# Performance work log

Hardware: AMD Instinct MI355X
Metric: run time of the kernel (lower is better)

## Reference

```python
import jax, jax.numpy as jnp
import numpy as np

N_NODES = 4096
IN_FEAT = 256
N_HEADS = 8
N_HIDDEN = 64  # out_features // n_heads
NEG_SLOPE = 0.2
EDGE_PROB = 0.05


def setup_inputs() -> dict:
    key = jax.random.key(0)
    k1, k2, k3, k4 = jax.random.split(key, 4)
    h = jax.random.normal(k1, (N_NODES, IN_FEAT), dtype=jnp.float32)
    # binary adjacency mask [N, N, 1] (broadcast over heads), as in the torch asserts
    adj_mat = (jax.random.uniform(k2, (N_NODES, N_NODES, 1)) < EDGE_PROB).astype(jnp.float32)
    # nn.Linear(in_features, n_heads*n_hidden, bias=False) weight: [H*F, in]
    W = jax.random.normal(k3, (N_HEADS * N_HIDDEN, IN_FEAT), dtype=jnp.float32) / np.sqrt(IN_FEAT)
    # nn.Linear(2*n_hidden, 1, bias=False) weight, flattened: [2*F]
    a = jax.random.normal(k4, (2 * N_HIDDEN,), dtype=jnp.float32) / np.sqrt(2 * N_HIDDEN)
    return {"h": h, "adj_mat": adj_mat, "W": W, "a": a}


def reference(h, adj_mat, W, a):
    n = h.shape[0]
    # g: [N, H, F]
    g = (h @ W.T).reshape(n, N_HEADS, N_HIDDEN)
    # attn(cat[g_i, g_j]) == a_l . g_i + a_r . g_j  (linear, no bias)
    a_l = a[:N_HIDDEN]
    a_r = a[N_HIDDEN:]
    el = jnp.einsum('ihf,f->ih', g, a_l)  # [N, H]
    er = jnp.einsum('jhf,f->jh', g, a_r)  # [N, H]
    e = jax.nn.leaky_relu(el[:, None, :] + er[None, :, :], NEG_SLOPE)  # [N, N, H]
    # note: original multiplies scores by adjacency (not masked_fill)
    e = e * adj_mat  # adj broadcasts over heads
    att = jax.nn.softmax(e, axis=1)  # softmax over source nodes j
    # dropout is identity at eval (dropout_rate=0.0)
    out = jnp.einsum('ijh,jhf->ihf', att, g)  # [N, H, F]
    return out.reshape(n, N_HEADS * N_HIDDEN)
```

## Files before the change

kernel.cpp:

```cpp
#include <hip/hip_runtime.h>

#define N_NODES 4096
#define IN_FEAT 256
#define N_HEADS 8
#define N_HIDDEN 64
#define OUT_FEAT (N_HEADS * N_HIDDEN)
#define NEG_SLOPE 0.2f

typedef _Float16 half8 __attribute__((ext_vector_type(8)));
typedef _Float16 h2 __attribute__((ext_vector_type(2)));
typedef float floatx4 __attribute__((ext_vector_type(4)));

__global__ __launch_bounds__(256) void produce(
    const float* __restrict__ H, const float* __restrict__ adj,
    const float* __restrict__ Wt, const float* __restrict__ a,
    _Float16* __restrict__ GT16, float* __restrict__ elT,
    _Float16* __restrict__ eR1h, _Float16* __restrict__ eR2h,
    unsigned long long* __restrict__ bits) {
  __shared__ _Float16 SM[4 * 64 * 64];
  const int t = threadIdx.x;
  const int bx = blockIdx.x, by = blockIdx.y;

  if (by >= 8) {
    const int c = bx * 8 + (by - 8);
    const size_t W0 = (size_t)c * 512;
    const int wv = t >> 6, lane = t & 63;
    for (int k0 = 0; k0 < 128; k0 += 8) {
      float v[8];
#pragma unroll
      for (int k = 0; k < 8; ++k)
        v[k] = adj[(W0 + wv * 128 + k0 + k) * 64 + lane];
#pragma unroll
      for (int k = 0; k < 8; ++k) {
        unsigned long long m = __ballot(v[k] != 0.f);
        if (lane == 0) bits[W0 + wv * 128 + k0 + k] = m;
      }
    }
    return;
  }

  _Float16* Ah = SM;
  _Float16* Al = SM + 4096;
  _Float16* Bh = SM + 8192;
  _Float16* Bl = SM + 12288;
  const int w = t >> 6, l = t & 63;
  const int n16 = l & 15, q = l >> 4;
  const int bi = bx, bo = by;
  const int m0 = bi * 64 + w * 16;

  floatx4 acc[4];
#pragma unroll
  for (int ct = 0; ct < 4; ++ct) acc[ct] = (floatx4)0.f;

  for (int kc = 0; kc < 4; ++kc) {
    if (kc) __syncthreads();
#pragma unroll
    for (int p = 0; p < 4; ++p) {
      const int idx = p * 256 + t;
      const int r = idx >> 4;
      const int c4 = (idx & 15) << 2;
      const int dst = r * 64 + ((((idx & 15) >> 1)) ^ (r & 7)) * 8 + (idx & 1) * 4;
      float4 hv = *(const float4*)(H + (size_t)(bi * 64 + r) * IN_FEAT + kc * 64 + c4);
      float4 wv = *(const float4*)(Wt + (size_t)(bo * 64 + r) * IN_FEAT + kc * 64 + c4);
      union { _Float16 h[4]; int2 d; } hh_, hl_, wh_, wl_;
      hh_.h[0] = (_Float16)hv.x; hh_.h[1] = (_Float16)hv.y;
      hh_.h[2] = (_Float16)hv.z; hh_.h[3] = (_Float16)hv.w;
      hl_.h[0] = (_Float16)(hv.x - (float)hh_.h[0]);
      hl_.h[1] = (_Float16)(hv.y - (float)hh_.h[1]);
      hl_.h[2] = (_Float16)(hv.z - (float)hh_.h[2]);
      hl_.h[3] = (_Float16)(hv.w - (float)hh_.h[3]);
      wh_.h[0] = (_Float16)wv.x; wh_.h[1] = (_Float16)wv.y;
      wh_.h[2] = (_Float16)wv.z; wh_.h[3] = (_Float16)wv.w;
      wl_.h[0] = (_Float16)(wv.x - (float)wh_.h[0]);
      wl_.h[1] = (_Float16)(wv.y - (float)wh_.h[1]);
      wl_.h[2] = (_Float16)(wv.z - (float)wh_.h[2]);
      wl_.h[3] = (_Float16)(wv.w - (float)wh_.h[3]);
      *(int2*)&Ah[dst] = hh_.d;
      *(int2*)&Al[dst] = hl_.d;
      *(int2*)&Bh[dst] = wh_.d;
      *(int2*)&Bl[dst] = wl_.d;
    }
    __syncthreads();
#pragma unroll
    for (int ks = 0; ks < 2; ++ks) {
      const int ao = (w * 16 + n16) * 64 + (((ks << 2) + q) ^ (n16 & 7)) * 8;
      half8 Afh = *(const half8*)&Ah[ao];
      half8 Afl = *(const half8*)&Al[ao];
#pragma unroll
      for (int ct = 0; ct < 4; ++ct) {
        const int bofs = (ct * 16 + n16) * 64 + (((ks << 2) + q) ^ (n16 & 7)) * 8;
        half8 Bfh = *(const half8*)&Bh[bofs];
        half8 Bfl = *(const half8*)&Bl[bofs];
        acc[ct] = __builtin_amdgcn_mfma_f32_16x16x32_f16(Afh, Bfh, acc[ct], 0, 0, 0);
        acc[ct] = __builtin_amdgcn_mfma_f32_16x16x32_f16(Afl, Bfh, acc[ct], 0, 0, 0);
        acc[ct] = __builtin_amdgcn_mfma_f32_16x16x32_f16(Afh, Bfl, acc[ct], 0, 0, 0);
      }
    }
  }

  float aLv[4], aRv[4];
#pragma unroll
  for (int ct = 0; ct < 4; ++ct) {
    aLv[ct] = a[ct * 16 + n16];
    aRv[ct] = a[64 + ct * 16 + n16];
  }
#pragma unroll
  for (int reg = 0; reg < 4; ++reg) {
    float sl = 0.f, sr = 0.f;
#pragma unroll
    for (int ct = 0; ct < 4; ++ct) {
      sl = fmaf(acc[ct][reg], aLv[ct], sl);
      sr = fmaf(acc[ct][reg], aRv[ct], sr);
    }
#pragma unroll
    for (int off = 1; off < 16; off <<= 1) {
      sl += __shfl_xor(sl, off);
      sr += __shfl_xor(sr, off);
    }
    if (n16 == 0) {
      const int rowi = m0 + q * 4 + reg;
      elT[(size_t)bo * N_NODES + rowi] = sl;
      eR1h[(size_t)bo * N_NODES + rowi] = (_Float16)__expf(sr);
      eR2h[(size_t)bo * N_NODES + rowi] = (_Float16)__expf(0.2f * sr);
    }
  }

  __syncthreads();
  _Float16* LG = SM;
#pragma unroll
  for (int ct = 0; ct < 4; ++ct)
#pragma unroll
    for (int reg = 0; reg < 4; ++reg)
      LG[(w * 16 + q * 4 + reg) * 72 + ct * 16 + n16] = (_Float16)acc[ct][reg];
  __syncthreads();
  {
    const int f = t >> 2, jq = t & 3;
    union { _Float16 hh[16]; int4 v[2]; } u;
#pragma unroll
    for (int k = 0; k < 16; ++k) u.hh[k] = LG[(jq * 16 + k) * 72 + f];
    _Float16* dst = GT16 + (size_t)(bo * 64 + f) * N_NODES + bi * 64 + jq * 16;
    *(int4*)dst = u.v[0];
    *(int4*)(dst + 8) = u.v[1];
  }
}

__global__ __launch_bounds__(256) void attn_v8(
    const unsigned long long* __restrict__ bits, const _Float16* __restrict__ GT16,
    const float* __restrict__ elT, const _Float16* __restrict__ eR1h,
    const _Float16* __restrict__ eR2h, float* __restrict__ out) {
  __shared__ __align__(16) _Float16 Gt[2][2][4096];
  __shared__ __align__(16) _Float16 eRs1[2][2][64];
  __shared__ __align__(16) _Float16 eRs2[2][2][64];
  __shared__ float eL1s[32], eL2s[32];
  __shared__ float Zh1[32], Zfull[32];

  const int t = threadIdx.x;
  const int ib = blockIdx.x, h = blockIdx.y;
  const int i0 = ib * 32;
  const int w = t >> 6, l = t & 63, n16 = l & 15, q = l >> 4;
  const int rt = w & 1, jh = w >> 1;

  const _Float16* gsrcs[4];
  int ldsbase[4];
#pragma unroll
  for (int c = 0; c < 4; ++c) {
    const int flat = w * 256 + c * 64 + l;
    const int fjh = flat >> 9;
    const int ff = (flat >> 3) & 63;
    const int ss = flat & 7;
    const int cg = ss ^ (ff & 7);
    gsrcs[c] = GT16 + (size_t)(h * 64 + ff) * N_NODES + fjh * 2048 + cg * 8;
    ldsbase[c] = (w * 256 + c * 64) * 8;
  }
  const int era = (t >> 3) & 1, erjh = t >> 4, erseg = t & 7;
  const _Float16* esrc0 = (era ? eR2h : eR1h) + (size_t)h * N_NODES + erjh * 2048 + erseg * 8;
  const unsigned long long* bp = bits + (size_t)(i0 + rt * 16 + n16) * 64 + jh * 32;

  if (t < 32) {
    float e = elT[(size_t)h * N_NODES + i0 + t];
    eL1s[t] = __expf(e);
    eL2s[t] = __expf(0.2f * e);
  }
#pragma unroll
  for (int c = 0; c < 4; ++c)
    __builtin_amdgcn_global_load_lds(
        (const __attribute__((address_space(1))) unsigned int*)gsrcs[c],
        (__attribute__((address_space(3))) unsigned int*)(&Gt[0][0][0] + ldsbase[c]),
        16, 0, 0);
  if (t < 32) {
    int4 ev = *(const int4*)esrc0;
    *(int4*)&(era ? eRs2 : eRs1)[0][erjh][erseg * 8] = ev;
  }
  unsigned long long bvc = bp[0];
  __syncthreads();

  const _Float16 e1f = (_Float16)eL1s[rt * 16 + n16];
  const _Float16 e2f = (_Float16)eL2s[rt * 16 + n16];
  const h2 eL1h2 = {e1f, e1f};
  const h2 eL2h2 = {e2f, e2f};
  half8 Bones;
#pragma unroll
  for (int k = 0; k < 8; ++k) Bones[k] = (n16 == 0) ? (_Float16)1.f : (_Float16)0.f;

  floatx4 acc[4];
#pragma unroll
  for (int ft = 0; ft < 4; ++ft) acc[ft] = (floatx4)0.f;
  floatx4 acc5 = (floatx4)0.f;

  int par = 0;
  for (int step = 0; step < 32; ++step) {
    int4 ev;
    unsigned long long bvn = bvc;
    if (step + 1 < 32) {
      const int np = par ^ 1;
#pragma unroll
      for (int c = 0; c < 4; ++c)
        __builtin_amdgcn_global_load_lds(
            (const __attribute__((address_space(1))) unsigned int*)(gsrcs[c] + (step + 1) * 64),
            (__attribute__((address_space(3))) unsigned int*)(&Gt[np][0][0] + ldsbase[c]),
            16, 0, 0);
      if (t < 32) ev = *(const int4*)(esrc0 + (step + 1) * 64);
      bvn = bp[step + 1];
    }
    const _Float16* gt = &Gt[par][jh][0];
#pragma unroll
    for (int ks = 0; ks < 2; ++ks) {
      const unsigned dw = (unsigned)(bvc >> (ks * 32));
      const unsigned byte = (dw >> (q * 8)) & 0xffu;
      uint4 r1 = *(const uint4*)&eRs1[par][jh][ks * 32 + q * 8];
      uint4 r2 = *(const uint4*)&eRs2[par][jh][ks * 32 + q * 8];
      const unsigned r1a[4] = {r1.x, r1.y, r1.z, r1.w};
      const unsigned r2a[4] = {r2.x, r2.y, r2.z, r2.w};
      unsigned pr[4];
#pragma unroll
      for (int kk = 0; kk < 4; ++kk) {
        h2 pa = eL1h2 * __builtin_bit_cast(h2, r1a[kk]);
        h2 pb = eL2h2 * __builtin_bit_cast(h2, r2a[kk]);
        h2 pv = __builtin_elementwise_max(pa, pb);
        unsigned y = (byte >> (2 * kk)) & 3u;
        unsigned b01 = (y | (y << 15)) & 0x00010001u;
        unsigned keep = b01 * 0xffffu;
        pr[kk] = (__builtin_bit_cast(unsigned, pv) & keep) | (0x3C003C00u & ~keep);
      }
      const uint4 prv = {pr[0], pr[1], pr[2], pr[3]};
      half8 Af = __builtin_bit_cast(half8, prv);
#pragma unroll
      for (int ft = 0; ft < 4; ++ft) {
        half8 Bf = *(const half8*)&gt[(ft * 16 + n16) * 64 + (((ks << 2) + q) ^ (n16 & 7)) * 8];
        acc[ft] = __builtin_amdgcn_mfma_f32_16x16x32_f16(Af, Bf, acc[ft], 0, 0, 0);
      }
      acc5 = __builtin_amdgcn_mfma_f32_16x16x32_f16(Af, Bones, acc5, 0, 0, 0);
    }
    if (step + 1 < 32 && t < 32)
      *(int4*)&(era ? eRs2 : eRs1)[par ^ 1][erjh][erseg * 8] = ev;
    bvc = bvn;
    __syncthreads();
    par ^= 1;
  }

  float* comb = (float*)&Gt[0][0][0];
  if (jh == 1) {
#pragma unroll
    for (int ft = 0; ft < 4; ++ft)
#pragma unroll
      for (int reg = 0; reg < 4; ++reg)
        comb[(rt * 16 + q * 4 + reg) * 68 + ft * 16 + n16] = acc[ft][reg];
    if (n16 == 0) {
#pragma unroll
      for (int reg = 0; reg < 4; ++reg) Zh1[rt * 16 + q * 4 + reg] = acc5[reg];
    }
  }
  __syncthreads();
  if (jh == 0) {
#pragma unroll
    for (int ft = 0; ft < 4; ++ft)
#pragma unroll
      for (int reg = 0; reg < 4; ++reg)
        acc[ft][reg] += comb[(rt * 16 + q * 4 + reg) * 68 + ft * 16 + n16];
    if (n16 == 0) {
#pragma unroll
      for (int reg = 0; reg < 4; ++reg) {
        const int row = rt * 16 + q * 4 + reg;
        Zfull[row] = acc5[reg] + Zh1[row];
      }
    }
  }
  __syncthreads();
  if (jh == 0) {
#pragma unroll
    for (int reg = 0; reg < 4; ++reg) {
      const int row = rt * 16 + q * 4 + reg;
      const float invz = 1.f / Zfull[row];
      float* op = out + (size_t)(i0 + row) * OUT_FEAT + h * 64;
#pragma unroll
      for (int ft = 0; ft < 4; ++ft) op[ft * 16 + n16] = acc[ft][reg] * invz;
    }
  }
}

extern "C" void kernel_launch(void* const* d_in, const int* in_sizes, int n_in,
                              void* d_out, int out_size, void* d_ws, size_t ws_size,
                              hipStream_t stream) {
  const float* h   = (const float*)d_in[0];
  const float* adj = (const float*)d_in[1];
  const float* W   = (const float*)d_in[2];
  const float* a   = (const float*)d_in[3];
  float* out = (float*)d_out;

  char* ws = (char*)d_ws;
  _Float16* GT16 = (_Float16*)ws;
  unsigned long long* bits = (unsigned long long*)(ws + 4u * 1024 * 1024);
  float* elT = (float*)(ws + 6u * 1024 * 1024);
  _Float16* eR1h = (_Float16*)(ws + 6u * 1024 * 1024 + 128 * 1024);
  _Float16* eR2h = (_Float16*)(ws + 6u * 1024 * 1024 + 192 * 1024);

  produce<<<dim3(64, 16), 256, 0, stream>>>(h, adj, W, a, GT16, elT, eR1h, eR2h, bits);
  attn_v8<<<dim3(128, 8), 256, 0, stream>>>(bits, GT16, elT, eR1h, eR2h, out);
}
```

Measured before the change: 157.4 us.

## Switch attention kernel to 32x32x16 MFMA with per-wave j-split and register eR

Rewrites the attention kernel so each of the four waves owns a quarter of the source-node range and covers all 32 rows, using 32x32x16 MFMA instead of 16x16x32 tiles. Right-side exponent values are now loaded straight into registers and double-buffered there, replacing the shared-memory staging. Partial sums from the four waves are reduced through LDS with a rotated layout, then written out as vectorized float4 stores. This aims to cut LDS reads of the B operand per MFMA and to shorten the epilogue. In exchange it needs more accumulator registers per wave and adds a four-way cross-wave reduction.

```diff
diff --git a/kernel.cpp b/kernel.cpp
--- a/kernel.cpp
+++ b/kernel.cpp
@@ -10,6 +10,8 @@
 typedef _Float16 half8 __attribute__((ext_vector_type(8)));
 typedef _Float16 h2 __attribute__((ext_vector_type(2)));
 typedef float floatx4 __attribute__((ext_vector_type(4)));
+typedef float floatx16 __attribute__((ext_vector_type(16)));
+typedef float f4 __attribute__((ext_vector_type(4)));
 
 __global__ __launch_bounds__(256) void produce(
     const float* __restrict__ H, const float* __restrict__ adj,
@@ -144,91 +146,92 @@
   }
 }
 
-__global__ __launch_bounds__(256) void attn_v8(
+__global__ __launch_bounds__(256, 4) void attn_v9(
     const unsigned long long* __restrict__ bits, const _Float16* __restrict__ GT16,
     const float* __restrict__ elT, const _Float16* __restrict__ eR1h,
     const _Float16* __restrict__ eR2h, float* __restrict__ out) {
-  __shared__ __align__(16) _Float16 Gt[2][2][4096];
-  __shared__ __align__(16) _Float16 eRs1[2][2][64];
-  __shared__ __align__(16) _Float16 eRs2[2][2][64];
+  __shared__ __align__(16) _Float16 Gt[2][4][2048];
   __shared__ float eL1s[32], eL2s[32];
-  __shared__ float Zh1[32], Zfull[32];
+  __shared__ float Zp[4][32];
 
   const int t = threadIdx.x;
   const int ib = blockIdx.x, h = blockIdx.y;
   const int i0 = ib * 32;
-  const int w = t >> 6, l = t & 63, n16 = l & 15, q = l >> 4;
-  const int rt = w & 1, jh = w >> 1;
+  const int w = t >> 6, l = t & 63;
+  const int c31 = l & 31, hi = l >> 5, hi8 = hi * 8;
 
   const _Float16* gsrcs[4];
-  int ldsbase[4];
 #pragma unroll
   for (int c = 0; c < 4; ++c) {
-    const int flat = w * 256 + c * 64 + l;
-    const int fjh = flat >> 9;
-    const int ff = (flat >> 3) & 63;
-    const int ss = flat & 7;
-    const int cg = ss ^ (ff & 7);
-    gsrcs[c] = GT16 + (size_t)(h * 64 + ff) * N_NODES + fjh * 2048 + cg * 8;
-    ldsbase[c] = (w * 256 + c * 64) * 8;
-  }
-  const int era = (t >> 3) & 1, erjh = t >> 4, erseg = t & 7;
-  const _Float16* esrc0 = (era ? eR2h : eR1h) + (size_t)h * N_NODES + erjh * 2048 + erseg * 8;
-  const unsigned long long* bp = bits + (size_t)(i0 + rt * 16 + n16) * 64 + jh * 32;
+    const int feat = c * 16 + (l >> 2);
+    const int p = l & 3;
+    gsrcs[c] = GT16 + (size_t)(h * 64 + feat) * N_NODES + w * 1024 + (p ^ (feat & 3)) * 8;
+  }
+
+  const _Float16* er1p = eR1h + (size_t)h * N_NODES + w * 1024 + hi8;
+  const _Float16* er2p = eR2h + (size_t)h * N_NODES + w * 1024 + hi8;
+  const unsigned* bp = (const unsigned*)bits + (size_t)(i0 + c31) * 128 + w * 32;
 
   if (t < 32) {
     float e = elT[(size_t)h * N_NODES + i0 + t];
     eL1s[t] = __expf(e);
     eL2s[t] = __expf(0.2f * e);
   }
+
 #pragma unroll
   for (int c = 0; c < 4; ++c)
     __builtin_amdgcn_global_load_lds(
         (const __attribute__((address_space(1))) unsigned int*)gsrcs[c],
-        (__attribute__((address_space(3))) unsigned int*)(&Gt[0][0][0] + ldsbase[c]),
+        (__attribute__((address_space(3))) unsigned int*)&Gt[0][w][c * 512],
         16, 0, 0);
-  if (t < 32) {
-    int4 ev = *(const int4*)esrc0;
-    *(int4*)&(era ? eRs2 : eRs1)[0][erjh][erseg * 8] = ev;
-  }
-  unsigned long long bvc = bp[0];
+  uint4 e1c0 = *(const uint4*)er1p;
+  uint4 e1c1 = *(const uint4*)(er1p + 16);
+  uint4 e2c0 = *(const uint4*)er2p;
+  uint4 e2c1 = *(const uint4*)(er2p + 16);
+  unsigned bvc = bp[0];
   __syncthreads();
 
-  const _Float16 e1f = (_Float16)eL1s[rt * 16 + n16];
-  const _Float16 e2f = (_Float16)eL2s[rt * 16 + n16];
+  const _Float16 e1f = (_Float16)eL1s[c31];
+  const _Float16 e2f = (_Float16)eL2s[c31];
   const h2 eL1h2 = {e1f, e1f};
   const h2 eL2h2 = {e2f, e2f};
   half8 Bones;
 #pragma unroll
-  for (int k = 0; k < 8; ++k) Bones[k] = (n16 == 0) ? (_Float16)1.f : (_Float16)0.f;
-
-  floatx4 acc[4];
-#pragma unroll
-  for (int ft = 0; ft < 4; ++ft) acc[ft] = (floatx4)0.f;
-  floatx4 acc5 = (floatx4)0.f;
+  for (int k = 0; k < 8; ++k) Bones[k] = (c31 == 0) ? (_Float16)1.f : (_Float16)0.f;
+
+  int boff[2][2];
+#pragma unroll
+  for (int ft = 0; ft < 2; ++ft)
+#pragma unroll
+    for (int ch = 0; ch < 2; ++ch)
+      boff[ft][ch] = (ft * 32 + c31) * 32 + (((ch * 2 + hi) ^ (c31 & 3)) * 8);
+
+  floatx16 acc0 = (floatx16)0.f, acc1 = (floatx16)0.f, accZ = (floatx16)0.f;
 
   int par = 0;
   for (int step = 0; step < 32; ++step) {
-    int4 ev;
-    unsigned long long bvn = bvc;
+    uint4 e1n0 = e1c0, e1n1 = e1c1, e2n0 = e2c0, e2n1 = e2c1;
+    unsigned bvn = bvc;
     if (step + 1 < 32) {
       const int np = par ^ 1;
 #pragma unroll
       for (int c = 0; c < 4; ++c)
         __builtin_amdgcn_global_load_lds(
-            (const __attribute__((address_space(1))) unsigned int*)(gsrcs[c] + (step + 1) * 64),
-            (__attribute__((address_space(3))) unsigned int*)(&Gt[np][0][0] + ldsbase[c]),
+            (const __attribute__((address_space(1))) unsigned int*)(gsrcs[c] + (step + 1) * 32),
+            (__attribute__((address_space(3))) unsigned int*)&Gt[np][w][c * 512],
             16, 0, 0);
-      if (t < 32) ev = *(const int4*)(esrc0 + (step + 1) * 64);
+      e1n0 = *(const uint4*)(er1p + (step + 1) * 32);
+      e1n1 = *(const uint4*)(er1p + (step + 1) * 32 + 16);
+      e2n0 = *(const uint4*)(er2p + (step + 1) * 32);
+      e2n1 = *(const uint4*)(er2p + (step + 1) * 32 + 16);
       bvn = bp[step + 1];
     }
-    const _Float16* gt = &Gt[par][jh][0];
-#pragma unroll
-    for (int ks = 0; ks < 2; ++ks) {
-      const unsigned dw = (unsigned)(bvc >> (ks * 32));
-      const unsigned byte = (dw >> (q * 8)) & 0xffu;
-      uint4 r1 = *(const uint4*)&eRs1[par][jh][ks * 32 + q * 8];
-      uint4 r2 = *(const uint4*)&eRs2[par][jh][ks * 32 + q * 8];
+    const _Float16* gt = &Gt[par][w][0];
+#pragma unroll
+    for (int ch = 0; ch < 2; ++ch) {
+      const unsigned byte = (bvc >> (ch * 16 + hi8)) & 0xffu;
+      const uint4 r1 = ch ? e1c1 : e1c0;
+      const uint4 r2 = ch ? e2c1 : e2c0;
       const unsigned r1a[4] = {r1.x, r1.y, r1.z, r1.w};
       const unsigned r2a[4] = {r2.x, r2.y, r2.z, r2.w};
       unsigned pr[4];
@@ -244,57 +247,50 @@
       }
       const uint4 prv = {pr[0], pr[1], pr[2], pr[3]};
       half8 Af = __builtin_bit_cast(half8, prv);
-#pragma unroll
-      for (int ft = 0; ft < 4; ++ft) {
-        half8 Bf = *(const half8*)&gt[(ft * 16 + n16) * 64 + (((ks << 2) + q) ^ (n16 & 7)) * 8];
-        acc[ft] = __builtin_amdgcn_mfma_f32_16x16x32_f16(Af, Bf, acc[ft], 0, 0, 0);
-      }
-      acc5 = __builtin_amdgcn_mfma_f32_16x16x32_f16(Af, Bones, acc5, 0, 0, 0);
-    }
-    if (step + 1 < 32 && t < 32)
-      *(int4*)&(era ? eRs2 : eRs1)[par ^ 1][erjh][erseg * 8] = ev;
-    bvc = bvn;
+      half8 B0 = *(const half8*)&gt[boff[0][ch]];
+      half8 B1 = *(const half8*)&gt[boff[1][ch]];
+      acc0 = __builtin_amdgcn_mfma_f32_32x32x16_f16(Af, B0, acc0, 0, 0, 0);
+      acc1 = __builtin_amdgcn_mfma_f32_32x32x16_f16(Af, B1, acc1, 0, 0, 0);
+      accZ = __builtin_amdgcn_mfma_f32_32x32x16_f16(Af, Bones, accZ, 0, 0, 0);
+    }
+    e1c0 = e1n0; e1c1 = e1n1; e2c0 = e2n0; e2c1 = e2n1; bvc = bvn;
     __syncthreads();
     par ^= 1;
   }
 
-  float* comb = (float*)&Gt[0][0][0];
-  if (jh == 1) {
-#pragma unroll
-    for (int ft = 0; ft < 4; ++ft)
-#pragma unroll
-      for (int reg = 0; reg < 4; ++reg)
-        comb[(rt * 16 + q * 4 + reg) * 68 + ft * 16 + n16] = acc[ft][reg];
-    if (n16 == 0) {
-#pragma unroll
-      for (int reg = 0; reg < 4; ++reg) Zh1[rt * 16 + q * 4 + reg] = acc5[reg];
-    }
+  float* sc = (float*)&Gt[0][0][0];
+#pragma unroll
+  for (int ft = 0; ft < 2; ++ft) {
+#pragma unroll
+    for (int r = 0; r < 16; ++r) {
+      const int row = (r & 3) + 8 * (r >> 2) + 4 * hi;
+      const int col = (ft * 32 + c31 + row * 4) & 63;
+      sc[w * 2048 + row * 64 + col] = ft ? acc1[r] : acc0[r];
+    }
+  }
+  if (c31 == 0) {
+#pragma unroll
+    for (int r = 0; r < 16; ++r)
+      Zp[w][(r & 3) + 8 * (r >> 2) + 4 * hi] = accZ[r];
   }
   __syncthreads();
-  if (jh == 0) {
-#pragma unroll
-    for (int ft = 0; ft < 4; ++ft)
-#pragma unroll
-      for (int reg = 0; reg < 4; ++reg)
-        acc[ft][reg] += comb[(rt * 16 + q * 4 + reg) * 68 + ft * 16 + n16];
-    if (n16 == 0) {
-#pragma unroll
-      for (int reg = 0; reg < 4; ++reg) {
-        const int row = rt * 16 + q * 4 + reg;
-        Zfull[row] = acc5[reg] + Zh1[row];
-      }
-    }
-  }
-  __syncthreads();
-  if (jh == 0) {
-#pragma unroll
-    for (int reg = 0; reg < 4; ++reg) {
-      const int row = rt * 16 + q * 4 + reg;
-      const float invz = 1.f / Zfull[row];
-      float* op = out + (size_t)(i0 + row) * OUT_FEAT + h * 64;
-#pragma unroll
-      for (int ft = 0; ft < 4; ++ft) op[ft * 16 + n16] = acc[ft][reg] * invz;
-    }
+  {
+    const int row = t >> 3, cg = (t & 7) * 8;
+    const int sA = (cg + row * 4) & 63;
+    const int sB = (cg + 4 + row * 4) & 63;
+    f4 s0 = (f4)0.f, s1 = (f4)0.f;
+#pragma unroll
+    for (int w4 = 0; w4 < 4; ++w4) {
+      s0 += *(const f4*)&sc[w4 * 2048 + row * 64 + sA];
+      s1 += *(const f4*)&sc[w4 * 2048 + row * 64 + sB];
+    }
+    const float Z = Zp[0][row] + Zp[1][row] + Zp[2][row] + Zp[3][row];
+    const float invz = 1.f / Z;
+    s0 *= invz;
+    s1 *= invz;
+    float* op = out + (size_t)(i0 + row) * OUT_FEAT + h * 64 + cg;
+    *(f4*)op = s0;
+    *(f4*)(op + 4) = s1;
   }
 }
 
@@ -315,5 +311,5 @@
   _Float16* eR2h = (_Float16*)(ws + 6u * 1024 * 1024 + 192 * 1024);
 
   produce<<<dim3(64, 16), 256, 0, stream>>>(h, adj, W, a, GT16, elT, eR1h, eR2h, bits);
-  attn_v8<<<dim3(128, 8), 256, 0, stream>>>(bits, GT16, elT, eR1h, eR2h, out);
+  attn_v9<<<dim3(128, 8), 256, 0, stream>>>(bits, GT16, elT, eR1h, eR2h, out);
 }
```

Measured after the change: 173.4 us. 10.1% more time.
